# Optimization experiments

Hardware: AMD Instinct MI355X
Metric: run time of the kernel (lower is better)

## Reference

```python
import jax, jax.numpy as jnp
import numpy as np

B, S = 16, 512
VD, TD, H, NH = 768, 768, 1024, 16
HD = H // NH
MAXREL = 128
THRESH = 2.0 / 3.0


def _bitlinear(x, W, b):
    # BitNet b1.58 eval-mode: ternary-quantize weights, rescale, dense matmul
    s = jnp.clip(jnp.mean(jnp.abs(W)), 1e-5, 1000.0)
    wn = jnp.clip(W / s, -10.0, 10.0)
    q = jnp.where(wn > THRESH, 1.0, jnp.where(wn < -THRESH, -1.0, 0.0))
    return x @ (q * s).T + b


def _ln(x, g, b, eps=1e-5):
    m = jnp.mean(x, axis=-1, keepdims=True)
    v = jnp.mean((x - m) ** 2, axis=-1, keepdims=True)
    return (x - m) * jax.lax.rsqrt(v + eps) * g + b


def setup_inputs() -> dict:
    key = jax.random.key(0)
    ks = jax.random.split(key, 10)
    def n(k, shape, std=0.02):
        return jax.random.normal(k, shape, dtype=jnp.float32) * std
    return dict(
        vision_features=jax.random.normal(ks[0], (B, VD), dtype=jnp.float32),
        text_features=jax.random.normal(ks[1], (B, S, TD), dtype=jnp.float32),
        W_vp=n(ks[2], (H, VD)), b_vp=jnp.zeros((H,), jnp.float32),
        W_tp=n(ks[3], (H, TD)), b_tp=jnp.zeros((H,), jnp.float32),
        W_tqkv=n(ks[4], (3 * H, H)), b_tqkv=jnp.zeros((3 * H,), jnp.float32),
        W_vout=n(ks[5], (H, H)), b_vout=jnp.zeros((H,), jnp.float32),
        W_tout=n(ks[6], (H, H)), b_tout=jnp.zeros((H,), jnp.float32),
        g_tn=jnp.ones((H,), jnp.float32), be_tn=jnp.zeros((H,), jnp.float32),
        g_i2t=jnp.ones((H,), jnp.float32), be_i2t=jnp.zeros((H,), jnp.float32),
        g_t2i=jnp.ones((H,), jnp.float32), be_t2i=jnp.zeros((H,), jnp.float32),
        alpha_i2t=jnp.zeros((1,), jnp.float32),
        alpha_t2i=jnp.zeros((1,), jnp.float32),
        rel_embed=n(ks[7], (2 * MAXREL + 1, NH)),
        text_mask=jnp.ones((B, S), dtype=bool),
    )


def reference(vision_features, text_features, W_vp, b_vp, W_tp, b_tp,
              W_tqkv, b_tqkv, W_vout, b_vout, W_tout, b_tout,
              g_tn, be_tn, g_i2t, be_i2t, g_t2i, be_t2i,
              alpha_i2t, alpha_t2i, rel_embed, text_mask):
    scale = HD ** -0.5
    vision_proj = _bitlinear(vision_features, W_vp, b_vp)            # [B,H]
    text_proj = _bitlinear(text_features, W_tp, b_tp)                # [B,S,H]

    # --- text self-attention with relative-position bias ---
    qkv = _bitlinear(_ln(text_proj, g_tn, be_tn), W_tqkv, b_tqkv)    # [B,S,3H]
    qkv = qkv.reshape(B, S, 3, NH, HD).transpose(2, 0, 3, 1, 4)      # [3,B,nh,S,hd]
    q, k, v = qkv[0], qkv[1], qkv[2]
    attn = jnp.einsum('bhqd,bhkd->bhqk', q, k) * scale
    coords = jnp.arange(S)
    rel = jnp.clip(coords[:, None] - coords[None, :], -MAXREL, MAXREL) + MAXREL
    attn = attn + rel_embed[rel].transpose(2, 0, 1)[None]            # +[1,nh,S,S]
    attn = jnp.where(text_mask[:, None, None, :], attn, -1e9)
    attn = jax.nn.softmax(attn, axis=-1)
    text_self = jnp.einsum('bhqk,bhkd->bhqd', attn, v)
    text_self = text_self.transpose(0, 2, 1, 3).reshape(B, S, H)
    text_self = text_proj + text_self                                # residual

    # --- image -> text cross-attention (vision token queries text) ---
    vq = jnp.broadcast_to(vision_proj[:, None], (B, S, H))
    vq = vq.reshape(B, S, NH, HD).transpose(0, 2, 1, 3)              # [B,nh,S,hd]
    tkv = text_self.reshape(B, S, NH, HD).transpose(0, 2, 1, 3)      # [B,nh,S,hd]
    i2t = jnp.einsum('bhqd,bhkd->bhqk', vq, tkv) * scale
    i2t = jnp.where(text_mask[:, None, None, :], i2t, -1e9)
    i2t = jax.nn.softmax(i2t, axis=-1)
    i2t_out = jnp.einsum('bhqk,bhkd->bhqd', i2t, tkv)
    i2t_out = i2t_out.transpose(0, 2, 1, 3).reshape(B, S, H).mean(axis=1)
    i2t_out = _ln(i2t_out, g_i2t, be_i2t)                            # [B,H]
    fused_vision = vision_proj + alpha_i2t * _bitlinear(i2t_out, W_vout, b_vout)

    # --- text -> image cross-attention (text queries single vision token) ---
    tq = text_self.reshape(B, S, NH, HD).transpose(0, 2, 1, 3)       # [B,nh,S,hd]
    vkv = vision_proj.reshape(B, 1, NH, HD).transpose(0, 2, 1, 3)    # [B,nh,1,hd]
    t2i = jnp.einsum('bhqd,bhkd->bhqk', tq, vkv) * scale             # [B,nh,S,1]
    t2i = jax.nn.softmax(t2i, axis=-1)
    t2i_out = jnp.einsum('bhqk,bhkd->bhqd', t2i, vkv)
    t2i_out = t2i_out.transpose(0, 2, 1, 3).reshape(B, S, H)
    t2i_out = _ln(t2i_out, g_t2i, be_t2i)
    fused_text = text_self + alpha_t2i * _bitlinear(t2i_out, W_tout, b_tout)

    return fused_vision, fused_text
```

## Files before the change

### kernel.cpp

```cpp
#include <hip/hip_runtime.h>
#include <cstdint>

#define B_   16
#define S_   512
#define VD_  768
#define TD_  768
#define H_   1024
#define NH_  16
#define HD_  64
#define H3_  3072

typedef __attribute__((ext_vector_type(8))) short bf16x8;
typedef __attribute__((ext_vector_type(4))) float f32x4;

__device__ __forceinline__ float b2f(unsigned short h) {
  union { unsigned u; float f; } x; x.u = ((unsigned)h) << 16; return x.f;
}
__device__ __forceinline__ unsigned short f2b(float f) {
  union { float f; unsigned u; } x; x.f = f;
  unsigned r = x.u + 0x7fffu + ((x.u >> 16) & 1u);
  return (unsigned short)(r >> 16);
}
__device__ __forceinline__ unsigned cvt_pk_bf16(float lo, float hi) {
  unsigned r;
  __asm__("v_cvt_pk_bf16_f32 %0, %1, %2" : "=v"(r) : "v"(lo), "v"(hi));
  return r;
}
__device__ __forceinline__ float fexp2(float x) {
#if __has_builtin(__builtin_amdgcn_exp2f)
  return __builtin_amdgcn_exp2f(x);
#else
  return exp2f(x);
#endif
}

__device__ __forceinline__ void gload_lds16(const void* g, void* lds) {
  __builtin_amdgcn_global_load_lds(
      (const __attribute__((address_space(1))) unsigned int*)g,
      (__attribute__((address_space(3))) unsigned int*)lds, 16, 0, 0);
}
__device__ __forceinline__ void lds_wave_fence() {
  __asm__ __volatile__("s_waitcnt lgkmcnt(0)" ::: "memory");
}

__global__ __launch_bounds__(256) void k_abssum_cvt(const float* __restrict__ w0, int n0,
                                                    const float* __restrict__ w1, int n1,
                                                    const float* __restrict__ w2, int n2,
                                                    const float* __restrict__ w3, int n3,
                                                    const float* __restrict__ w4, int n4,
                                                    double* __restrict__ partials,
                                                    const float* __restrict__ cvt_in,
                                                    unsigned short* __restrict__ cvt_out,
                                                    int cvt_n4) {
  int y = blockIdx.y;
  if (y == 5) {
    for (int i = blockIdx.x * 256 + threadIdx.x; i < cvt_n4; i += 128 * 256) {
      float4 v = ((const float4*)cvt_in)[i];
      ushort4 o; o.x = f2b(v.x); o.y = f2b(v.y); o.z = f2b(v.z); o.w = f2b(v.w);
      ((ushort4*)cvt_out)[i] = o;
    }
    return;
  }
  const float* w = y == 0 ? w0 : y == 1 ? w1 : y == 2 ? w2 : y == 3 ? w3 : w4;
  int n4q = (y == 0 ? n0 : y == 1 ? n1 : y == 2 ? n2 : y == 3 ? n3 : n4) >> 2;
  double s = 0.0;
  for (int i = blockIdx.x * 256 + threadIdx.x; i < n4q; i += 128 * 256) {
    float4 v = ((const float4*)w)[i];
    s += (double)fabsf(v.x) + (double)fabsf(v.y) + (double)fabsf(v.z) + (double)fabsf(v.w);
  }
#pragma unroll
  for (int off = 32; off > 0; off >>= 1) s += __shfl_down(s, off, 64);
  __shared__ double red[4];
  if ((threadIdx.x & 63) == 0) red[threadIdx.x >> 6] = s;
  __syncthreads();
  if (threadIdx.x == 0)
    partials[y * 128 + blockIdx.x] = red[0] + red[1] + red[2] + red[3];
}

__global__ __launch_bounds__(512) void k_sumfin(const double* __restrict__ partials,
                                                double* __restrict__ sums) {
  int wave = threadIdx.x >> 6, lane = threadIdx.x & 63;
  if (wave >= 5) return;
  double s = partials[wave * 128 + lane] + partials[wave * 128 + 64 + lane];
#pragma unroll
  for (int off = 32; off > 0; off >>= 1) s += __shfl_down(s, off, 64);
  if (lane == 0) sums[wave] = s;
}

__global__ __launch_bounds__(256) void k_quant5(const float* __restrict__ w0, int n0,
                                                const float* __restrict__ w1, int n1,
                                                const float* __restrict__ w2, int n2,
                                                const float* __restrict__ w3, int n3,
                                                const float* __restrict__ w4, int n4,
                                                unsigned short* __restrict__ q0,
                                                unsigned short* __restrict__ q1,
                                                unsigned short* __restrict__ q2,
                                                unsigned short* __restrict__ q3,
                                                unsigned short* __restrict__ q4,
                                                const double* __restrict__ sum,
                                                float* __restrict__ s_out) {
  int y = blockIdx.y;
  const float* w = y == 0 ? w0 : y == 1 ? w1 : y == 2 ? w2 : y == 3 ? w3 : w4;
  unsigned short* q = y == 0 ? q0 : y == 1 ? q1 : y == 2 ? q2 : y == 3 ? q3 : q4;
  int n = y == 0 ? n0 : y == 1 ? n1 : y == 2 ? n2 : y == 3 ? n3 : n4;
  double s = fmin(fmax(sum[y] / (double)n, 1e-5), 1000.0);
  if (blockIdx.x == 0 && threadIdx.x == 0) s_out[y] = (float)s;
  int i = blockIdx.x * 256 + threadIdx.x;
  if (i < n) {
    double wn = (double)w[i] / s;
    unsigned short o = 0;
    if (wn > (2.0 / 3.0)) o = 0x3F80u;
    else if (wn < -(2.0 / 3.0)) o = 0xBF80u;
    q[i] = o;
  }
}

__global__ __launch_bounds__(256) void k_rowmat(const float* __restrict__ A,
                                                const unsigned short* __restrict__ W,
                                                const float* __restrict__ sptr,
                                                const float* __restrict__ bias,
                                                float* __restrict__ Cf,
                                                unsigned short* __restrict__ Cb,
                                                const float* __restrict__ resid,
                                                const float* __restrict__ alpha,
                                                int N, int K) {
  const int t = threadIdx.x, lane = t & 63;
  const int w_idx = blockIdx.x * 4 + (t >> 6);
  const int m = w_idx / N, n = w_idx - m * N;
  const int Kper = K >> 6;
  const float* a = A + (size_t)m * K + lane * Kper;
  const unsigned short* w = W + (size_t)n * K + lane * Kper;
  float acc = 0.f;
  for (int k = 0; k < Kper; k += 4) {
    float4 av = *(const float4*)(a + k);
    ushort4 wv = *(const ushort4*)(w + k);
    acc += av.x * b2f(wv.x) + av.y * b2f(wv.y) + av.z * b2f(wv.z) + av.w * b2f(wv.w);
  }
#pragma unroll
  for (int off = 32; off > 0; off >>= 1) acc += __shfl_down(acc, off, 64);
  if (lane == 0) {
    float v = acc * sptr[0] + bias[n];
    if (resid) v = resid[w_idx] + alpha[0] * v;
    Cf[w_idx] = v;
    if (Cb) Cb[w_idx] = f2b(v);
  }
}

__global__ __launch_bounds__(256) void k_ln(const float* __restrict__ x,
                                            const float* __restrict__ g,
                                            const float* __restrict__ be,
                                            float* __restrict__ of,
                                            unsigned short* __restrict__ ob) {
  int row = blockIdx.x, t = threadIdx.x;
  const float4* xr = (const float4*)(x + (size_t)row * H_);
  float4 v = xr[t];
  float s = v.x + v.y + v.z + v.w;
  float s2 = v.x * v.x + v.y * v.y + v.z * v.z + v.w * v.w;
#pragma unroll
  for (int off = 32; off > 0; off >>= 1) { s += __shfl_down(s, off, 64); s2 += __shfl_down(s2, off, 64); }
  __shared__ float rs[4], rs2[4];
  if ((t & 63) == 0) { rs[t >> 6] = s; rs2[t >> 6] = s2; }
  __syncthreads();
  s = rs[0] + rs[1] + rs[2] + rs[3];
  s2 = rs2[0] + rs2[1] + rs2[2] + rs2[3];
  float mean = s * (1.0f / H_);
  float var = s2 * (1.0f / H_) - mean * mean;
  float rstd = rsqrtf(var + 1e-5f);
  const float4 gv = ((const float4*)g)[t];
  const float4 bv = ((const float4*)be)[t];
  float4 o;
  o.x = (v.x - mean) * rstd * gv.x + bv.x;
  o.y = (v.y - mean) * rstd * gv.y + bv.y;
  o.z = (v.z - mean) * rstd * gv.z + bv.z;
  o.w = (v.w - mean) * rstd * gv.w + bv.w;
  if (of) ((float4*)(of + (size_t)row * H_))[t] = o;
  if (ob) {
    ushort4 ou; ou.x = f2b(o.x); ou.y = f2b(o.y); ou.z = f2b(o.z); ou.w = f2b(o.w);
    ((ushort4*)(ob + (size_t)row * H_))[t] = ou;
  }
}

template <int OUTB, int VT>
__global__ __launch_bounds__(256) void k_gemm(const unsigned short* __restrict__ A,
                                              const unsigned short* __restrict__ W,
                                              const float* __restrict__ sptr,
                                              const float* __restrict__ bias,
                                              float* __restrict__ Cf,
                                              unsigned short* __restrict__ Cb,
                                              unsigned short* __restrict__ vt,
                                              int M, int N, int K) {
  __shared__ __align__(16) unsigned short As[2][128 * 32];
  __shared__ __align__(16) unsigned short Bs[2][128 * 32];
  const int t = threadIdx.x, wave = t >> 6, lane = t & 63, quad = lane >> 4, l16 = lane & 15;
  const int bm = blockIdx.y * 128, bn = blockIdx.x * 128;
  const int wm = (wave >> 1) * 64, wn = (wave & 1) * 64;
  f32x4 acc[4][4];
#pragma unroll
  for (int i = 0; i < 4; ++i)
#pragma unroll
    for (int j = 0; j < 4; ++j) acc[i][j] = f32x4{0.f, 0.f, 0.f, 0.f};

  const int srow = lane >> 2, skc = lane & 3;
  auto stage = [&](int k0, int buf) {
#pragma unroll
    for (int c = 0; c < 2; ++c) {
      int row = (wave * 2 + c) * 16 + srow;
      gload_lds16(A + (size_t)(bm + row) * K + k0 + skc * 8, &As[buf][(wave * 2 + c) * 512]);
      gload_lds16(W + (size_t)(bn + row) * K + k0 + skc * 8, &Bs[buf][(wave * 2 + c) * 512]);
    }
  };

  stage(0, 0);
  int it = 0;
  for (int k0 = 0; k0 < K; k0 += 32, ++it) {
    const int cur = it & 1;
    __syncthreads();
    if (k0 + 32 < K) stage(k0 + 32, cur ^ 1);
    bf16x8 af[4], bfrg[4];
#pragma unroll
    for (int i = 0; i < 4; ++i)
      af[i] = *(const bf16x8*)&As[cur][(wm + i * 16 + l16) * 32 + quad * 8];
#pragma unroll
    for (int j = 0; j < 4; ++j)
      bfrg[j] = *(const bf16x8*)&Bs[cur][(wn + j * 16 + l16) * 32 + quad * 8];
#pragma unroll
    for (int i = 0; i < 4; ++i)
#pragma unroll
      for (int j = 0; j < 4; ++j)
        acc[i][j] = __builtin_amdgcn_mfma_f32_16x16x32_bf16(af[i], bfrg[j], acc[i][j], 0, 0, 0);
  }
  float s = sptr[0];

  if (VT && bn >= 2 * H_) {
    __syncthreads();
    unsigned short* T = (wave < 2) ? &As[0][wave * 1152] : &Bs[0][(wave - 2) * 1152];
    const int h = (bn + wn - 2 * H_) >> 6;
    const int b = (bm + wm) >> 9, s0 = (bm + wm) & (S_ - 1);
    const int chunk0 = lane * 2;
#pragma unroll
    for (int j = 0; j < 4; ++j) {
      int n = bn + wn + j * 16 + l16;
      float bv = bias[n];
#pragma unroll
      for (int i = 0; i < 4; ++i)
#pragma unroll
        for (int r = 0; r < 4; ++r)
          T[l16 * 72 + i * 16 + quad * 4 + r] = f2b(acc[i][j][r] * s + bv);
      lds_wave_fence();
#pragma unroll
      for (int cc = 0; cc < 2; ++cc) {
        int ch = chunk0 + cc, dr = ch >> 3, k8 = ch & 7;
        uint4 val = *(const uint4*)&T[dr * 72 + k8 * 8];
        *(uint4*)(vt + ((size_t)(b * NH_ + h) * HD_ + j * 16 + dr) * S_ + s0 + k8 * 8) = val;
      }
      lds_wave_fence();
    }
    return;
  }

#pragma unroll
  for (int j = 0; j < 4; ++j) {
    int n = bn + wn + j * 16 + l16;
    float bv = bias[n];
#pragma unroll
    for (int i = 0; i < 4; ++i) {
#pragma unroll
      for (int r = 0; r < 4; ++r) {
        int m = bm + wm + i * 16 + quad * 4 + r;
        float v = acc[i][j][r] * s + bv;
        if (OUTB) Cb[(size_t)m * N + n] = f2b(v);
        else      Cf[(size_t)m * N + n] = v;
      }
    }
  }
}

__global__ __launch_bounds__(256) void k_flash(const unsigned short* __restrict__ qkv,
                                               const unsigned short* __restrict__ vt,
                                               const float* __restrict__ tp,
                                               const float* __restrict__ rel,
                                               const float* __restrict__ trow,
                                               const float* __restrict__ a_t2i,
                                               float* __restrict__ out_text,
                                               unsigned short* __restrict__ ts_b) {
  const int qt = blockIdx.x, h = blockIdx.y, b = blockIdx.z;
  __shared__ __align__(16) unsigned short Qs[64 * 64];
  __shared__ __align__(16) unsigned short Ks[2][64 * 64];
  __shared__ __align__(16) unsigned short Vs[2][64 * 64];
  __shared__ __align__(16) unsigned short Ps[4][16 * 72];
  __shared__ float rels[257];
  const int t = threadIdx.x, wave = t >> 6, lane = t & 63, quad = lane >> 4, l16 = lane & 15;
  const int srow = lane >> 3;
  const int kcg = (lane & 7) ^ srow;
  const float LOG2E = 1.4426950408889634f;
  const float SC = 0.125f * LOG2E;

  for (int i = t; i < 257; i += 256) rels[i] = rel[i * NH_ + h] * LOG2E;

  auto stage_kv = [&](int kt, int buf) {
#pragma unroll
    for (int c = 0; c < 2; ++c) {
      int row = (wave * 2 + c) * 8 + srow;
      gload_lds16(qkv + (size_t)(b * S_ + kt * 64 + row) * H3_ + H_ + h * HD_ + kcg * 8,
                  &Ks[buf][(wave * 2 + c) * 512]);
      gload_lds16(vt + ((size_t)(b * NH_ + h) * HD_ + row) * S_ + kt * 64 + kcg * 8,
                  &Vs[buf][(wave * 2 + c) * 512]);
    }
  };

#pragma unroll
  for (int c = 0; c < 2; ++c) {
    int row = (wave * 2 + c) * 8 + srow;
    gload_lds16(qkv + (size_t)(b * S_ + qt * 64 + row) * H3_ + h * HD_ + kcg * 8,
                &Qs[(wave * 2 + c) * 512]);
  }
  stage_kv(0, 0);

  float mrun = -1e30f, lrun = 0.f;
  f32x4 o[4];
#pragma unroll
  for (int j = 0; j < 4; ++j) o[j] = f32x4{0.f, 0.f, 0.f, 0.f};

  bf16x8 aq0, aq1;
  bool qloaded = false;
  const int qg = qt * 64 + wave * 16 + l16;

  for (int kt = 0; kt < 8; ++kt) {
    const int cur = kt & 1;
    __syncthreads();
    if (kt < 7) stage_kv(kt + 1, cur ^ 1);

    if (!qloaded) {
      int R = wave * 16 + l16;
      aq0 = *(const bf16x8*)&Qs[R * 64 + ((quad ^ (R & 7)) * 8)];
      aq1 = *(const bf16x8*)&Qs[R * 64 + (((4 + quad) ^ (R & 7)) * 8)];
      qloaded = true;
    }

    const int dq = qt - kt;
    const bool uni = (dq >= 3) || (dq <= -3);
    const float bu = uni ? rels[dq >= 3 ? 256 : 0] : 0.f;

    float pv[4][4];
#pragma unroll
    for (int j = 0; j < 4; ++j) {
      int R = j * 16 + l16;
      bf16x8 kb0 = *(const bf16x8*)&Ks[cur][R * 64 + ((quad ^ (R & 7)) * 8)];
      bf16x8 kb1 = *(const bf16x8*)&Ks[cur][R * 64 + (((4 + quad) ^ (R & 7)) * 8)];
      f32x4 z = f32x4{0.f, 0.f, 0.f, 0.f};
      z = __builtin_amdgcn_mfma_f32_16x16x32_bf16(kb0, aq0, z, 0, 0, 0);
      z = __builtin_amdgcn_mfma_f32_16x16x32_bf16(kb1, aq1, z, 0, 0, 0);
      if (uni) {
#pragma unroll
        for (int r = 0; r < 4; ++r) pv[j][r] = z[r] * SC + bu;
      } else {
        const int kg0 = kt * 64 + j * 16 + quad * 4;
#pragma unroll
        for (int r = 0; r < 4; ++r) {
          int rix = min(max(qg - kg0 - r, -128), 128) + 128;
          pv[j][r] = z[r] * SC + rels[rix];
        }
      }
    }
    float x = pv[0][0];
#pragma unroll
    for (int j = 0; j < 4; ++j)
#pragma unroll
      for (int r = 0; r < 4; ++r) x = fmaxf(x, pv[j][r]);
    x = fmaxf(x, __shfl_xor(x, 16, 64));
    x = fmaxf(x, __shfl_xor(x, 32, 64));
    if (!__all(x <= mrun)) {
      float mn = fmaxf(mrun, x);
      float al = fexp2(mrun - mn);
      mrun = mn;
      lrun *= al;
      float al0 = __shfl(al, quad * 4 + 0, 64);
      float al1 = __shfl(al, quad * 4 + 1, 64);
      float al2 = __shfl(al, quad * 4 + 2, 64);
      float al3 = __shfl(al, quad * 4 + 3, 64);
#pragma unroll
      for (int jd = 0; jd < 4; ++jd) {
        o[jd][0] *= al0; o[jd][1] *= al1; o[jd][2] *= al2; o[jd][3] *= al3;
      }
    }
    float rsum = 0.f;
#pragma unroll
    for (int j = 0; j < 4; ++j)
#pragma unroll
      for (int r = 0; r < 4; ++r) {
        float p = fexp2(pv[j][r] - mrun);
        pv[j][r] = p;
        rsum += p;
      }
    rsum += __shfl_xor(rsum, 16, 64);
    rsum += __shfl_xor(rsum, 32, 64);
    lrun += rsum;
    unsigned char* psb = (unsigned char*)&Ps[wave][0] + l16 * 144 + quad * 8;
#pragma unroll
    for (int j = 0; j < 4; ++j) {
      uint2 pk;
      pk.x = cvt_pk_bf16(pv[j][0], pv[j][1]);
      pk.y = cvt_pk_bf16(pv[j][2], pv[j][3]);
      *(uint2*)(psb + j * 32) = pk;
    }
    lds_wave_fence();
#pragma unroll
    for (int ks = 0; ks < 2; ++ks) {
      bf16x8 ap = *(const bf16x8*)&Ps[wave][l16 * 72 + ks * 32 + quad * 8];
#pragma unroll
      for (int jd = 0; jd < 4; ++jd) {
        int R = jd * 16 + l16;
        int C = ks * 4 + quad;
        bf16x8 vb = *(const bf16x8*)&Vs[cur][R * 64 + ((C ^ (R & 7)) * 8)];
        o[jd] = __builtin_amdgcn_mfma_f32_16x16x32_bf16(ap, vb, o[jd], 0, 0, 0);
      }
    }
  }
  float a2 = a_t2i[0];
  float il[4];
#pragma unroll
  for (int r = 0; r < 4; ++r) {
    float lr = __shfl(lrun, quad * 4 + r, 64);
    il[r] = 1.0f / lr;
  }
#pragma unroll
  for (int jd = 0; jd < 4; ++jd) {
#pragma unroll
    for (int r = 0; r < 4; ++r) {
      int g = b * S_ + qt * 64 + wave * 16 + quad * 4 + r;
      int col = h * HD_ + jd * 16 + l16;
      float ov = o[jd][r] * il[r];
      float ts = tp[(size_t)g * H_ + col] + ov;
      ts_b[(size_t)g * H_ + col] = f2b(ts);
      out_text[(size_t)g * H_ + col] = ts + a2 * trow[b * H_ + col];
    }
  }
}

__global__ __launch_bounds__(256) void k_i2t(const unsigned short* __restrict__ vp_b,
                                             const unsigned short* __restrict__ ts_b,
                                             float* __restrict__ i2t_out) {
  const int h = blockIdx.x & 15, b = blockIdx.x >> 4;
  __shared__ float sc[512];
  __shared__ float red[4];
  __shared__ float qv[64];
  __shared__ float ored[4][64];
  const int t = threadIdx.x;
  if (t < 64) qv[t] = b2f(vp_b[b * H_ + h * HD_ + t]);
  __syncthreads();
  for (int k = t; k < 512; k += 256) {
    const unsigned short* kr = ts_b + (size_t)(b * S_ + k) * H_ + h * HD_;
    float acc = 0.f;
#pragma unroll
    for (int dc = 0; dc < 8; ++dc) {
      uint4 u = *(const uint4*)(kr + dc * 8);
      const unsigned short* p = (const unsigned short*)&u;
#pragma unroll
      for (int i = 0; i < 8; ++i) acc += qv[dc * 8 + i] * b2f(p[i]);
    }
    sc[k] = acc * 0.125f;
  }
  __syncthreads();
  float m = -1e30f;
  for (int k = t; k < 512; k += 256) m = fmaxf(m, sc[k]);
#pragma unroll
  for (int off = 1; off < 64; off <<= 1) m = fmaxf(m, __shfl_xor(m, off, 64));
  if ((t & 63) == 0) red[t >> 6] = m;
  __syncthreads();
  m = fmaxf(fmaxf(red[0], red[1]), fmaxf(red[2], red[3]));
  __syncthreads();
  float ls = 0.f;
  for (int k = t; k < 512; k += 256) { float p = __expf(sc[k] - m); sc[k] = p; ls += p; }
#pragma unroll
  for (int off = 1; off < 64; off <<= 1) ls += __shfl_xor(ls, off, 64);
  if ((t & 63) == 0) red[t >> 6] = ls;
  __syncthreads();
  float tot = red[0] + red[1] + red[2] + red[3];
  const int d = t & 63, grp = t >> 6;
  float acc = 0.f;
  for (int k = grp; k < 512; k += 4)
    acc += sc[k] * b2f(ts_b[(size_t)(b * S_ + k) * H_ + h * HD_ + d]);
  ored[grp][d] = acc;
  __syncthreads();
  if (t < 64)
    i2t_out[b * H_ + h * HD_ + t] = (ored[0][t] + ored[1][t] + ored[2][t] + ored[3][t]) / tot;
}

extern "C" void kernel_launch(void* const* d_in, const int* in_sizes, int n_in,
                              void* d_out, int out_size, void* d_ws, size_t ws_size,
                              hipStream_t stream) {
  const float* vf     = (const float*)d_in[0];
  const float* tf     = (const float*)d_in[1];
  const float* W_vp   = (const float*)d_in[2];
  const float* b_vp   = (const float*)d_in[3];
  const float* W_tp   = (const float*)d_in[4];
  const float* b_tp   = (const float*)d_in[5];
  const float* W_tqkv = (const float*)d_in[6];
  const float* b_tqkv = (const float*)d_in[7];
  const float* W_vout = (const float*)d_in[8];
  const float* b_vout = (const float*)d_in[9];
  const float* W_tout = (const float*)d_in[10];
  const float* b_tout = (const float*)d_in[11];
  const float* g_tn   = (const float*)d_in[12];
  const float* be_tn  = (const float*)d_in[13];
  const float* g_i2t  = (const float*)d_in[14];
  const float* be_i2t = (const float*)d_in[15];
  const float* g_t2i  = (const float*)d_in[16];
  const float* be_t2i = (const float*)d_in[17];
  const float* a_i2t  = (const float*)d_in[18];
  const float* a_t2i  = (const float*)d_in[19];
  const float* rel    = (const float*)d_in[20];

  size_t off = 0;
  auto alloc = [&](size_t bytes) -> void* {
    void* p = (char*)d_ws + off;
    off += (bytes + 255) & ~(size_t)255;
    return p;
  };
  double* sums     = (double*)alloc(64);
  double* partials = (double*)alloc(5 * 128 * 8);
  float* scales    = (float*)alloc(64);
  unsigned short* q_vp   = (unsigned short*)alloc((size_t)H_ * VD_ * 2);
  unsigned short* q_tp   = (unsigned short*)alloc((size_t)H_ * TD_ * 2);
  unsigned short* q_tqkv = (unsigned short*)alloc((size_t)H3_ * H_ * 2);
  unsigned short* q_vout = (unsigned short*)alloc((size_t)H_ * H_ * 2);
  unsigned short* q_tout = (unsigned short*)alloc((size_t)H_ * H_ * 2);
  unsigned short* tf_b   = (unsigned short*)alloc((size_t)B_ * S_ * TD_ * 2);
  float* text_proj       = (float*)alloc((size_t)B_ * S_ * H_ * 4);
  unsigned short* ln_tp  = (unsigned short*)alloc((size_t)B_ * S_ * H_ * 2);
  unsigned short* qkv    = (unsigned short*)alloc((size_t)B_ * S_ * H3_ * 2);
  unsigned short* vt     = (unsigned short*)alloc((size_t)B_ * NH_ * HD_ * S_ * 2);
  unsigned short* ts_b   = (unsigned short*)alloc((size_t)B_ * S_ * H_ * 2);
  float* vision_proj     = (float*)alloc((size_t)B_ * H_ * 4);
  unsigned short* vp_b   = (unsigned short*)alloc((size_t)B_ * H_ * 2);
  float* ln_t2i_f        = (float*)alloc((size_t)B_ * H_ * 4);
  float* trow            = (float*)alloc((size_t)B_ * H_ * 4);
  float* i2t_out         = (float*)alloc((size_t)B_ * H_ * 4);
  float* ln_i2t_f        = (float*)alloc((size_t)B_ * H_ * 4);

  float* out_vision = (float*)d_out;
  float* out_text   = (float*)d_out + B_ * H_;

  k_abssum_cvt<<<dim3(128, 6), 256, 0, stream>>>(W_vp, H_ * VD_, W_tp, H_ * TD_,
                                                 W_tqkv, H3_ * H_, W_vout, H_ * H_,
                                                 W_tout, H_ * H_, partials,
                                                 tf, tf_b, B_ * S_ * TD_ / 4);
  k_sumfin<<<1, 512, 0, stream>>>(partials, sums);
  k_quant5<<<dim3((H3_ * H_ + 255) / 256, 5), 256, 0, stream>>>(
      W_vp, H_ * VD_, W_tp, H_ * TD_, W_tqkv, H3_ * H_, W_vout, H_ * H_, W_tout, H_ * H_,
      q_vp, q_tp, q_tqkv, q_vout, q_tout, sums, scales);

  k_rowmat<<<(B_ * H_) / 4, 256, 0, stream>>>(vf, q_vp, scales + 0, b_vp,
                                              vision_proj, vp_b, nullptr, nullptr, H_, VD_);
  k_ln<<<B_, 256, 0, stream>>>(vision_proj, g_t2i, be_t2i, ln_t2i_f, nullptr);
  k_rowmat<<<(B_ * H_) / 4, 256, 0, stream>>>(ln_t2i_f, q_tout, scales + 4, b_tout,
                                              trow, nullptr, nullptr, nullptr, H_, H_);

  k_gemm<0, 0><<<dim3(H_ / 128, (B_ * S_) / 128), 256, 0, stream>>>(
      tf_b, q_tp, scales + 1, b_tp, text_proj, nullptr, nullptr, B_ * S_, H_, TD_);
  k_ln<<<B_ * S_, 256, 0, stream>>>(text_proj, g_tn, be_tn, nullptr, ln_tp);
  k_gemm<1, 1><<<dim3(H3_ / 128, (B_ * S_) / 128), 256, 0, stream>>>(
      ln_tp, q_tqkv, scales + 2, b_tqkv, nullptr, qkv, vt, B_ * S_, H3_, H_);
  k_flash<<<dim3(S_ / 64, NH_, B_), 256, 0, stream>>>(qkv, vt, text_proj, rel, trow, a_t2i,
                                                      out_text, ts_b);
  k_i2t<<<B_ * NH_, 256, 0, stream>>>(vp_b, ts_b, i2t_out);
  k_ln<<<B_, 256, 0, stream>>>(i2t_out, g_i2t, be_i2t, ln_i2t_f, nullptr);
  k_rowmat<<<(B_ * H_) / 4, 256, 0, stream>>>(ln_i2t_f, q_vout, scales + 3, b_vout,
                                              out_vision, nullptr, vision_proj, a_i2t, H_, H_);
}
```

Measured before the change: 392.8 us.

## Enlarge GEMM tiles to 128x256 with triple-buffered swizzled LDS pipeline

Reworks the bf16 MFMA GEMM to use 512 threads on a 128x256 output tile with a 64-wide K step. It triple-buffers the LDS stages and waits with explicit vmcnt counts so loads run two tiles ahead. An XOR swizzle on LDS column chunks avoids bank conflicts, and s_setprio raises priority around the MFMA bursts. LDS use grows to about 144KB per block, which lowers occupancy and leaves fewer blocks for the grid, and the hand-written waitcnt counts must match the number of issued loads.

Measured after the change: 397.0 us. Within noise of the previous version (+1.1%).

```diff
diff --git a/kernel.cpp b/kernel.cpp
--- a/kernel.cpp
+++ b/kernel.cpp
@@ -181,7 +181,7 @@
 }
 
 template <int OUTB, int VT>
-__global__ __launch_bounds__(256) void k_gemm(const unsigned short* __restrict__ A,
+__global__ __launch_bounds__(512) void k_gemm(const unsigned short* __restrict__ A,
                                               const unsigned short* __restrict__ W,
                                               const float* __restrict__ sptr,
                                               const float* __restrict__ bias,
@@ -189,51 +189,72 @@
                                               unsigned short* __restrict__ Cb,
                                               unsigned short* __restrict__ vt,
                                               int M, int N, int K) {
-  __shared__ __align__(16) unsigned short As[2][128 * 32];
-  __shared__ __align__(16) unsigned short Bs[2][128 * 32];
+  __shared__ __align__(16) unsigned short As[3][128 * 64];
+  __shared__ __align__(16) unsigned short Bs[3][256 * 64];
   const int t = threadIdx.x, wave = t >> 6, lane = t & 63, quad = lane >> 4, l16 = lane & 15;
-  const int bm = blockIdx.y * 128, bn = blockIdx.x * 128;
-  const int wm = (wave >> 1) * 64, wn = (wave & 1) * 64;
+  const int bm = blockIdx.y * 128, bn = blockIdx.x * 256;
+  const int wm = (wave >> 2) * 64, wn = (wave & 3) * 64;
   f32x4 acc[4][4];
 #pragma unroll
   for (int i = 0; i < 4; ++i)
 #pragma unroll
     for (int j = 0; j < 4; ++j) acc[i][j] = f32x4{0.f, 0.f, 0.f, 0.f};
 
-  const int srow = lane >> 2, skc = lane & 3;
-  auto stage = [&](int k0, int buf) {
+  const int srow = lane >> 3;
+  const int kcg = (lane & 7) ^ srow;
+  auto stage = [&](int kt, int buf) {
+    const int k0 = kt * 64;
 #pragma unroll
     for (int c = 0; c < 2; ++c) {
-      int row = (wave * 2 + c) * 16 + srow;
-      gload_lds16(A + (size_t)(bm + row) * K + k0 + skc * 8, &As[buf][(wave * 2 + c) * 512]);
-      gload_lds16(W + (size_t)(bn + row) * K + k0 + skc * 8, &Bs[buf][(wave * 2 + c) * 512]);
+      int row = c * 64 + wave * 8 + srow;
+      gload_lds16(A + (size_t)(bm + row) * K + k0 + kcg * 8,
+                  &As[buf][(c * 64 + wave * 8) * 64]);
+    }
+#pragma unroll
+    for (int c = 0; c < 4; ++c) {
+      int row = c * 64 + wave * 8 + srow;
+      gload_lds16(W + (size_t)(bn + row) * K + k0 + kcg * 8,
+                  &Bs[buf][(c * 64 + wave * 8) * 64]);
     }
   };
 
+  const int NT = K >> 6;
   stage(0, 0);
-  int it = 0;
-  for (int k0 = 0; k0 < K; k0 += 32, ++it) {
-    const int cur = it & 1;
-    __syncthreads();
-    if (k0 + 32 < K) stage(k0 + 32, cur ^ 1);
-    bf16x8 af[4], bfrg[4];
-#pragma unroll
-    for (int i = 0; i < 4; ++i)
-      af[i] = *(const bf16x8*)&As[cur][(wm + i * 16 + l16) * 32 + quad * 8];
-#pragma unroll
-    for (int j = 0; j < 4; ++j)
-      bfrg[j] = *(const bf16x8*)&Bs[cur][(wn + j * 16 + l16) * 32 + quad * 8];
-#pragma unroll
-    for (int i = 0; i < 4; ++i)
-#pragma unroll
-      for (int j = 0; j < 4; ++j)
-        acc[i][j] = __builtin_amdgcn_mfma_f32_16x16x32_bf16(af[i], bfrg[j], acc[i][j], 0, 0, 0);
+  stage(1, 1);
+  for (int kt = 0; kt < NT; ++kt) {
+    if (kt + 1 < NT) __asm__ __volatile__("s_waitcnt vmcnt(6)" ::: "memory");
+    else             __asm__ __volatile__("s_waitcnt vmcnt(0)" ::: "memory");
+    __asm__ __volatile__("s_barrier" ::: "memory");
+    if (kt + 2 < NT) stage(kt + 2, (kt + 2) % 3);
+    const unsigned short* Ab = &As[kt % 3][0];
+    const unsigned short* Bb = &Bs[kt % 3][0];
+#pragma unroll
+    for (int ks = 0; ks < 2; ++ks) {
+      bf16x8 af[4], bfr[4];
+#pragma unroll
+      for (int i = 0; i < 4; ++i) {
+        int R = wm + i * 16 + l16;
+        af[i] = *(const bf16x8*)&Ab[R * 64 + (((ks * 4 + quad) ^ (R & 7)) * 8)];
+      }
+#pragma unroll
+      for (int j = 0; j < 4; ++j) {
+        int R = wn + j * 16 + l16;
+        bfr[j] = *(const bf16x8*)&Bb[R * 64 + (((ks * 4 + quad) ^ (R & 7)) * 8)];
+      }
+      __builtin_amdgcn_s_setprio(1);
+#pragma unroll
+      for (int i = 0; i < 4; ++i)
+#pragma unroll
+        for (int j = 0; j < 4; ++j)
+          acc[i][j] = __builtin_amdgcn_mfma_f32_16x16x32_bf16(af[i], bfr[j], acc[i][j], 0, 0, 0);
+      __builtin_amdgcn_s_setprio(0);
+    }
   }
   float s = sptr[0];
 
   if (VT && bn >= 2 * H_) {
     __syncthreads();
-    unsigned short* T = (wave < 2) ? &As[0][wave * 1152] : &Bs[0][(wave - 2) * 1152];
+    unsigned short* T = &As[0][0] + wave * 1152;
     const int h = (bn + wn - 2 * H_) >> 6;
     const int b = (bm + wm) >> 9, s0 = (bm + wm) & (S_ - 1);
     const int chunk0 = lane * 2;
@@ -556,10 +577,10 @@
   k_rowmat<<<(B_ * H_) / 4, 256, 0, stream>>>(ln_t2i_f, q_tout, scales + 4, b_tout,
                                               trow, nullptr, nullptr, nullptr, H_, H_);
 
-  k_gemm<0, 0><<<dim3(H_ / 128, (B_ * S_) / 128), 256, 0, stream>>>(
+  k_gemm<0, 0><<<dim3(H_ / 256, (B_ * S_) / 128), 512, 0, stream>>>(
       tf_b, q_tp, scales + 1, b_tp, text_proj, nullptr, nullptr, B_ * S_, H_, TD_);
   k_ln<<<B_ * S_, 256, 0, stream>>>(text_proj, g_tn, be_tn, nullptr, ln_tp);
-  k_gemm<1, 1><<<dim3(H3_ / 128, (B_ * S_) / 128), 256, 0, stream>>>(
+  k_gemm<1, 1><<<dim3(H3_ / 256, (B_ * S_) / 128), 512, 0, stream>>>(
       ln_tp, q_tqkv, scales + 2, b_tqkv, nullptr, qkv, vt, B_ * S_, H3_, H_);
   k_flash<<<dim3(S_ / 64, NH_, B_), 256, 0, stream>>>(qkv, vt, text_proj, rel, trow, a_t2i,
                                                       out_text, ts_b);
```

## Deepen GEMM K-tile to 64 with XOR-swizzled LDS and explicit vmcnt pipelining

Applied to the files above, without the earlier changes.

The bf16 MFMA GEMM now stages 64-wide K tiles instead of 32, halving the number of barrier iterations. It uses an XOR swizzle on the LDS layout to avoid bank conflicts on fragment reads. It also replaces __syncthreads with explicit s_waitcnt vmcnt and s_barrier so the next tile's global-to-LDS loads stay in flight during compute, and raises wave priority around MFMA issue. LDS use doubles, which may lower occupancy, and the hand-written waitcnt counts are fragile.

Result: faster. 376.6 us (-4.1%).

```diff
diff --git a/kernel.cpp b/kernel.cpp
--- a/kernel.cpp
+++ b/kernel.cpp
@@ -189,50 +189,67 @@
                                               unsigned short* __restrict__ Cb,
                                               unsigned short* __restrict__ vt,
                                               int M, int N, int K) {
-  __shared__ __align__(16) unsigned short As[2][128 * 32];
-  __shared__ __align__(16) unsigned short Bs[2][128 * 32];
+  __shared__ __align__(16) unsigned short As[2][128 * 64];
+  __shared__ __align__(16) unsigned short Bs[2][128 * 64];
   const int t = threadIdx.x, wave = t >> 6, lane = t & 63, quad = lane >> 4, l16 = lane & 15;
   const int bm = blockIdx.y * 128, bn = blockIdx.x * 128;
   const int wm = (wave >> 1) * 64, wn = (wave & 1) * 64;
+  const int srow = lane >> 3, kc = (lane & 7) ^ srow;
   f32x4 acc[4][4];
 #pragma unroll
   for (int i = 0; i < 4; ++i)
 #pragma unroll
     for (int j = 0; j < 4; ++j) acc[i][j] = f32x4{0.f, 0.f, 0.f, 0.f};
 
-  const int srow = lane >> 2, skc = lane & 3;
-  auto stage = [&](int k0, int buf) {
-#pragma unroll
-    for (int c = 0; c < 2; ++c) {
-      int row = (wave * 2 + c) * 16 + srow;
-      gload_lds16(A + (size_t)(bm + row) * K + k0 + skc * 8, &As[buf][(wave * 2 + c) * 512]);
-      gload_lds16(W + (size_t)(bn + row) * K + k0 + skc * 8, &Bs[buf][(wave * 2 + c) * 512]);
+  auto stage = [&](int kt, int buf) {
+    const int k0 = kt * 64;
+#pragma unroll
+    for (int c = 0; c < 4; ++c) {
+      int row = wave * 32 + c * 8 + srow;
+      gload_lds16(A + (size_t)(bm + row) * K + k0 + kc * 8,
+                  &As[buf][(wave * 32 + c * 8) * 64]);
+      gload_lds16(W + (size_t)(bn + row) * K + k0 + kc * 8,
+                  &Bs[buf][(wave * 32 + c * 8) * 64]);
     }
   };
 
+  const int NT = K >> 6;
   stage(0, 0);
-  int it = 0;
-  for (int k0 = 0; k0 < K; k0 += 32, ++it) {
-    const int cur = it & 1;
-    __syncthreads();
-    if (k0 + 32 < K) stage(k0 + 32, cur ^ 1);
-    bf16x8 af[4], bfrg[4];
-#pragma unroll
-    for (int i = 0; i < 4; ++i)
-      af[i] = *(const bf16x8*)&As[cur][(wm + i * 16 + l16) * 32 + quad * 8];
-#pragma unroll
-    for (int j = 0; j < 4; ++j)
-      bfrg[j] = *(const bf16x8*)&Bs[cur][(wn + j * 16 + l16) * 32 + quad * 8];
-#pragma unroll
-    for (int i = 0; i < 4; ++i)
-#pragma unroll
-      for (int j = 0; j < 4; ++j)
-        acc[i][j] = __builtin_amdgcn_mfma_f32_16x16x32_bf16(af[i], bfrg[j], acc[i][j], 0, 0, 0);
+  for (int kt = 0; kt < NT; ++kt) {
+    const int cur = kt & 1;
+    if (kt + 1 < NT) {
+      stage(kt + 1, cur ^ 1);
+      __asm__ __volatile__("s_waitcnt vmcnt(8)" ::: "memory");
+    } else {
+      __asm__ __volatile__("s_waitcnt vmcnt(0)" ::: "memory");
+    }
+    __asm__ __volatile__("s_barrier" ::: "memory");
+#pragma unroll
+    for (int ks = 0; ks < 2; ++ks) {
+      bf16x8 af[4], bfrg[4];
+#pragma unroll
+      for (int i = 0; i < 4; ++i) {
+        int R = wm + i * 16 + l16;
+        af[i] = *(const bf16x8*)&As[cur][R * 64 + (((ks * 4 + quad) ^ (R & 7)) * 8)];
+      }
+#pragma unroll
+      for (int j = 0; j < 4; ++j) {
+        int R = wn + j * 16 + l16;
+        bfrg[j] = *(const bf16x8*)&Bs[cur][R * 64 + (((ks * 4 + quad) ^ (R & 7)) * 8)];
+      }
+      __builtin_amdgcn_s_setprio(1);
+#pragma unroll
+      for (int i = 0; i < 4; ++i)
+#pragma unroll
+        for (int j = 0; j < 4; ++j)
+          acc[i][j] = __builtin_amdgcn_mfma_f32_16x16x32_bf16(af[i], bfrg[j], acc[i][j], 0, 0, 0);
+      __builtin_amdgcn_s_setprio(0);
+    }
+    __asm__ __volatile__("s_barrier" ::: "memory");
   }
   float s = sptr[0];
 
   if (VT && bn >= 2 * H_) {
-    __syncthreads();
     unsigned short* T = (wave < 2) ? &As[0][wave * 1152] : &Bs[0][(wave - 2) * 1152];
     const int h = (bn + wn - 2 * H_) >> 6;
     const int b = (bm + wm) >> 9, s0 = (bm + wm) & (S_ - 1);
```
